# Kernel optimization log

Hardware: AMD Instinct MI355X
Metric: run time of the kernel (lower is better)

Reference implementation:

```python
import jax, jax.numpy as jnp
import numpy as np

B, T, D, H = 8, 4096, 1024, 1024


def log_g(x):
    # log of g(x) = relu(x)+0.5 for x>=0, sigmoid(x) for x<0 (continuous at 0)
    return jnp.where(x >= 0, jnp.log(jax.nn.relu(x) + 0.5), -jax.nn.softplus(-x))


def setup_inputs() -> dict:
    key = jax.random.key(0)
    k0, k1, k2, k3, k4, k5 = jax.random.split(key, 6)
    s = 1.0 / np.sqrt(D)
    return {
        "x": jax.random.normal(k0, (B, T, D), jnp.float32),
        "h_0": jax.random.normal(k1, (B, H), jnp.float32),
        "Wz": jax.random.uniform(k2, (H, D), jnp.float32, -s, s),
        "bz": jax.random.uniform(k3, (H,), jnp.float32, -s, s),
        "Wh": jax.random.uniform(k4, (H, D), jnp.float32, -s, s),
        "bh": jax.random.uniform(k5, (H,), jnp.float32, -s, s),
    }


def reference(x, h_0, Wz, bz, Wh, bh):
    # gate pre-activation k: (B,T,H)
    k = jnp.einsum("btd,hd->bth", x, Wz) + bz
    log_z = -jax.nn.softplus(-k)        # log sigmoid(k)
    log_coeffs = -jax.nn.softplus(k)    # log (1 - sigmoid(k))
    log_h_0 = log_g(h_0)[:, None, :]    # (B,1,H)
    log_tilde_h = log_g(jnp.einsum("btd,hd->bth", x, Wh) + bh)
    log_values = jnp.concatenate([log_h_0, log_z + log_tilde_h], axis=1)  # (B,T+1,H)
    # parallel scan in log space
    a_star = jnp.pad(jnp.cumsum(log_coeffs, axis=1), ((0, 0), (1, 0), (0, 0)))
    log_h = a_star + jax.lax.cumlogsumexp(log_values - a_star, axis=1)
    h = jnp.exp(log_h)                  # (B,T+1,H)
    return h[:, -T:, :]
```

## Files before the change

### kernel.cpp

```cpp
#include <hip/hip_runtime.h>
#include <hip/hip_bf16.h>

#define Bb 8
#define Tt 4096
#define Dd 1024
#define Hh 1024
#define Mm (Bb * Tt)
#define NCHUNK 32
#define CLEN 128

typedef float f32x4 __attribute__((ext_vector_type(4)));
typedef short bf16x8 __attribute__((ext_vector_type(8)));

__device__ __forceinline__ unsigned f2bfu(float x) {
  unsigned u = __float_as_uint(x);
  return (u + 0x7fffu + ((u >> 16) & 1u)) >> 16;
}
__device__ __forceinline__ float bflo(unsigned u) { return __uint_as_float(u << 16); }
__device__ __forceinline__ float bfhi(unsigned u) { return __uint_as_float(u & 0xffff0000u); }

#define NX4 (Mm * Dd / 4)
#define NW4 (Hh * Dd / 4)
__global__ void cvt_all_kernel(const float* __restrict__ x,
                               const float* __restrict__ wz,
                               const float* __restrict__ wh,
                               unsigned short* __restrict__ xb,
                               unsigned short* __restrict__ wzb,
                               unsigned short* __restrict__ whb) {
  const int n4 = NX4 + 2 * NW4;
  int i = blockIdx.x * blockDim.x + threadIdx.x;
  const int stride = gridDim.x * blockDim.x;
  for (; i < n4; i += stride) {
    const float* src;
    unsigned short* dst;
    int j = i;
    if (j < NX4) {
      src = x; dst = xb;
    } else if (j < NX4 + NW4) {
      j -= NX4; src = wz; dst = wzb;
    } else {
      j -= NX4 + NW4; src = wh; dst = whb;
    }
    float4 v = reinterpret_cast<const float4*>(src)[j];
    ushort4 o;
    o.x = (unsigned short)f2bfu(v.x);
    o.y = (unsigned short)f2bfu(v.y);
    o.z = (unsigned short)f2bfu(v.z);
    o.w = (unsigned short)f2bfu(v.w);
    reinterpret_cast<ushort4*>(dst)[j] = o;
  }
}

__device__ __forceinline__ void async16(const unsigned short* g, unsigned short* l) {
  __builtin_amdgcn_global_load_lds(
      (const __attribute__((address_space(1))) unsigned int*)g,
      (__attribute__((address_space(3))) unsigned int*)l, 16, 0, 0);
}

#define SHFL_COMPOSE(A, Q, MASK, HIBIT)                                   \
  {                                                                       \
    const float pA_ = __shfl_xor(A, MASK);                                \
    const float pQ_ = __shfl_xor(Q, MASK);                                \
    const float Alo_ = (HIBIT) ? pA_ : A;                                 \
    const float Qlo_ = (HIBIT) ? pQ_ : Q;                                 \
    const float Ahi_ = (HIBIT) ? A : pA_;                                 \
    const float Qhi_ = (HIBIT) ? Q : pQ_;                                 \
    A = Alo_ * Ahi_;                                                      \
    Q = fmaf(Ahi_, Qlo_, Qhi_);                                           \
  }

__global__ void __launch_bounds__(512, 4) gemm_kernel(
    const unsigned short* __restrict__ xb,
    const unsigned short* __restrict__ wzb,
    const unsigned short* __restrict__ whb,
    const float* __restrict__ bz,
    const float* __restrict__ bh,
    unsigned int* __restrict__ P,
    float* __restrict__ Pp, float* __restrict__ Qq) {
  __shared__ unsigned short lds[36864];
  const int tid = threadIdx.x;
  const int wid = tid >> 6;
  const int wm = wid >> 2;
  const int wn = wid & 3;
  const int l = tid & 63, ln = l & 15, l4 = l >> 4;

  const int id = blockIdx.x;
  const int sw = (id & 7) * 256 + (id >> 3);
  const int mb = sw >> 3, nb = sw & 7;
  const int m0 = mb * 128, h0 = nb * 128;

  const int r0 = tid >> 2;
  const int chunk = ((tid & 3) - (tid >> 3)) & 3;
  const unsigned short* agp = xb + (size_t)(m0 + r0) * Dd + chunk * 8;
  const int sub16 = r0 >> 4;
  const int hrow0 = h0 + ((sub16 >> 1) << 4) + (r0 & 15);
  const unsigned short* bgp =
      ((sub16 & 1) ? whb : wzb) + (size_t)hrow0 * Dd + chunk * 8;
  const int ta = tid * 8;

  auto stage = [&](int buf) {
    unsigned short* d = &lds[buf * 12288];
    async16(agp, d + ta);
    async16(bgp, d + 4096 + ta);
    async16(bgp + (size_t)64 * Dd, d + 8192 + ta);
    agp += 32;
    bgp += 32;
  };

  int oA[4], oB[4];
#pragma unroll
  for (int mf = 0; mf < 4; ++mf) {
    const int row = wm * 64 + mf * 16 + ln;
    const int sl = (l4 + (row >> 1)) & 3;
    oA[mf] = row * 32 + sl * 8;
  }
#pragma unroll
  for (int nf = 0; nf < 4; ++nf) {
    const int row = wn * 64 + nf * 16 + ln;
    const int sl = (l4 + (row >> 1)) & 3;
    oB[nf] = 4096 + row * 32 + sl * 8;
  }

  f32x4 acc[4][4];
#pragma unroll
  for (int i = 0; i < 4; ++i)
#pragma unroll
    for (int j = 0; j < 4; ++j) acc[i][j] = f32x4{0.f, 0.f, 0.f, 0.f};

  stage(0);
  stage(1);

  int cur = 0, nxt = 2;
#pragma unroll 1
  for (int s = 0; s < 32; ++s) {
    asm volatile("s_waitcnt vmcnt(3)" ::: "memory");
    __builtin_amdgcn_s_barrier();
    const unsigned short* bp = &lds[cur * 12288];
    bf16x8 af[4], bf[4];
    af[0] = *(const bf16x8*)(bp + oA[0]);
    af[1] = *(const bf16x8*)(bp + oA[1]);
    af[2] = *(const bf16x8*)(bp + oA[2]);
    af[3] = *(const bf16x8*)(bp + oA[3]);
    bf[0] = *(const bf16x8*)(bp + oB[0]);
    bf[1] = *(const bf16x8*)(bp + oB[1]);
    bf[2] = *(const bf16x8*)(bp + oB[2]);
    bf[3] = *(const bf16x8*)(bp + oB[3]);
    stage(nxt);
    __builtin_amdgcn_s_setprio(1);
#pragma unroll
    for (int i = 0; i < 4; ++i)
#pragma unroll
      for (int j = 0; j < 4; ++j)
        acc[i][j] =
            __builtin_amdgcn_mfma_f32_16x16x32_bf16(af[i], bf[j], acc[i][j], 0, 0, 0);
    __builtin_amdgcn_s_setprio(0);
    cur = (cur + 1) == 3 ? 0 : cur + 1;
    nxt = (nxt + 1) == 3 ? 0 : nxt + 1;
  }

  asm volatile("s_waitcnt vmcnt(0)" ::: "memory");
  __syncthreads();

  float* sA = (float*)lds;
  float* sQ = (float*)lds + 256;
  const int b_idx = mb >> 5;
  const int ch = mb & 31;

#pragma unroll
  for (int p = 0; p < 2; ++p) {
    const int hcol = h0 + (wn * 2 + p) * 16 + ln;
    const float bzv = bz[hcol];
    const float bhv = bh[hcol];
    float Ar = 1.f, Qr = 0.f;
#pragma unroll
    for (int mf = 0; mf < 4; ++mf) {
      float A4 = 1.f, Q4 = 0.f;
#pragma unroll
      for (int q = 0; q < 4; ++q) {
        const int m = m0 + wm * 64 + mf * 16 + l4 * 4 + q;
        const float kv = acc[mf][2 * p][q] + bzv;
        const float pv = acc[mf][2 * p + 1][q] + bhv;
        const float ek = __expf(kv);
        const float a = 1.f / (1.f + ek);
        const float z = 1.f - a;
        const float g = (pv >= 0.f) ? (pv + 0.5f) : (1.f / (1.f + __expf(-pv)));
        const float c = z * g;
        const unsigned pw = f2bfu(a) | (f2bfu(c) << 16);
        P[(size_t)m * Hh + hcol] = pw;
        const float ar = bflo(pw), cr = bfhi(pw);
        Q4 = fmaf(ar, Q4, cr);
        A4 *= ar;
      }
      SHFL_COMPOSE(A4, Q4, 16, (l4 & 1));
      SHFL_COMPOSE(A4, Q4, 32, ((l4 >> 1) & 1));
      Qr = fmaf(A4, Qr, Q4);
      Ar *= A4;
    }
    if (l4 == 0) {
      sA[wm * 128 + (wn * 2 + p) * 16 + ln] = Ar;
      sQ[wm * 128 + (wn * 2 + p) * 16 + ln] = Qr;
    }
  }
  __syncthreads();
  if (tid < 128) {
    const float A0 = sA[tid], Q0 = sQ[tid];
    const float A1 = sA[128 + tid], Q1 = sQ[128 + tid];
    const int idx = ch * (Bb * Hh) + b_idx * Hh + (h0 + tid);
    Pp[idx] = A0 * A1;
    Qq[idx] = fmaf(A1, Q0, Q1);
  }
}

__global__ void scan_pass2(const float* __restrict__ h0raw,
                           const float* __restrict__ Pp, const float* __restrict__ Qq,
                           float* __restrict__ Hinit) {
  const int bh = blockIdx.x * 256 + threadIdx.x;
  const float x = h0raw[bh];
  float hs = (x >= 0.f) ? (x + 0.5f) : (1.f / (1.f + __expf(-x)));
  for (int ch = 0; ch < NCHUNK; ++ch) {
    const int idx = ch * (Bb * Hh) + bh;
    Hinit[idx] = hs;
    hs = fmaf(Pp[idx], hs, Qq[idx]);
  }
}

__global__ void scan_pass3(const unsigned int* __restrict__ P,
                           const float* __restrict__ Hinit,
                           float* __restrict__ out) {
  const int h = blockIdx.x * 256 + threadIdx.x;
  const int ch = blockIdx.y;
  const int b = blockIdx.z;
  float hs = Hinit[ch * (Bb * Hh) + b * Hh + h];
  const size_t base = ((size_t)(b * Tt + ch * CLEN)) * Hh + h;
  const unsigned int* p = P + base;
  float* o = out + base;
#pragma unroll 8
  for (int i = 0; i < CLEN; ++i) {
    const unsigned u = p[(size_t)i * Hh];
    hs = fmaf(bflo(u), hs, bfhi(u));
    o[(size_t)i * Hh] = hs;
  }
}

extern "C" void kernel_launch(void* const* d_in, const int* in_sizes, int n_in,
                              void* d_out, int out_size, void* d_ws, size_t ws_size,
                              hipStream_t stream) {
  const float* x  = (const float*)d_in[0];
  const float* h0 = (const float*)d_in[1];
  const float* Wz = (const float*)d_in[2];
  const float* bz = (const float*)d_in[3];
  const float* Wh = (const float*)d_in[4];
  const float* bh = (const float*)d_in[5];
  float* out = (float*)d_out;

  char* ws = (char*)d_ws;
  unsigned short* xb  = (unsigned short*)(ws);
  unsigned short* wzb = (unsigned short*)(ws + 67108864);
  unsigned short* whb = (unsigned short*)(ws + 69206016);
  unsigned int*   P   = (unsigned int*)(ws + 71303168);
  float* Pp    = (float*)(ws + 205520896);
  float* Qq    = (float*)(ws + 206569472);
  float* Hinit = (float*)(ws + 207618048);

  cvt_all_kernel<<<4096, 256, 0, stream>>>(x, Wz, Wh, xb, wzb, whb);

  gemm_kernel<<<2048, 512, 0, stream>>>(xb, wzb, whb, bz, bh, P, Pp, Qq);

  scan_pass2<<<Bb * Hh / 256, 256, 0, stream>>>(h0, Pp, Qq, Hinit);
  dim3 sgrid(Hh / 256, NCHUNK, Bb);
  scan_pass3<<<sgrid, 256, 0, stream>>>(P, Hinit, out);
}
```

Before: 260.0 us.

## Fuse fp32-to-bf16 conversion of x into GEMM A-tile loading

Removes the separate conversion pass over x (128MB read plus 64MB bf16 write) and instead has the GEMM load fp32 x tiles into registers, convert them to bf16 and write them to LDS, while B tiles keep the async global-to-LDS path. Only the weights are converted in a small pre-kernel. The trade-off is that the GEMM now reads twice the A bytes (each fp32 x tile is read once per N-block, 8 times over), spends more VGPRs on in-flight loads (launch bounds lowered to 3 waves/SIMD), and adds register-staged LDS writes with waitcnt ordering in the main loop. At the tail the loop issues dummy loads from the first tile so the vmcnt accounting stays consistent.

```diff
diff --git a/kernel.cpp b/kernel.cpp
--- a/kernel.cpp
+++ b/kernel.cpp
@@ -19,28 +19,18 @@
 __device__ __forceinline__ float bflo(unsigned u) { return __uint_as_float(u << 16); }
 __device__ __forceinline__ float bfhi(unsigned u) { return __uint_as_float(u & 0xffff0000u); }
 
-#define NX4 (Mm * Dd / 4)
 #define NW4 (Hh * Dd / 4)
-__global__ void cvt_all_kernel(const float* __restrict__ x,
-                               const float* __restrict__ wz,
-                               const float* __restrict__ wh,
-                               unsigned short* __restrict__ xb,
-                               unsigned short* __restrict__ wzb,
-                               unsigned short* __restrict__ whb) {
-  const int n4 = NX4 + 2 * NW4;
+__global__ void cvt_w_kernel(const float* __restrict__ wz,
+                             const float* __restrict__ wh,
+                             unsigned short* __restrict__ wzb,
+                             unsigned short* __restrict__ whb) {
+  const int n4 = 2 * NW4;
   int i = blockIdx.x * blockDim.x + threadIdx.x;
   const int stride = gridDim.x * blockDim.x;
   for (; i < n4; i += stride) {
-    const float* src;
-    unsigned short* dst;
-    int j = i;
-    if (j < NX4) {
-      src = x; dst = xb;
-    } else if (j < NX4 + NW4) {
-      j -= NX4; src = wz; dst = wzb;
-    } else {
-      j -= NX4 + NW4; src = wh; dst = whb;
-    }
+    const float* src = (i < NW4) ? wz : wh;
+    unsigned short* dst = (i < NW4) ? wzb : whb;
+    const int j = (i < NW4) ? i : i - NW4;
     float4 v = reinterpret_cast<const float4*>(src)[j];
     ushort4 o;
     o.x = (unsigned short)f2bfu(v.x);
@@ -69,8 +59,8 @@
     Q = fmaf(Ahi_, Qlo_, Qhi_);                                           \
   }
 
-__global__ void __launch_bounds__(512, 4) gemm_kernel(
-    const unsigned short* __restrict__ xb,
+__global__ void __launch_bounds__(512, 3) gemm_kernel(
+    const float* __restrict__ x,
     const unsigned short* __restrict__ wzb,
     const unsigned short* __restrict__ whb,
     const float* __restrict__ bz,
@@ -91,20 +81,27 @@
 
   const int r0 = tid >> 2;
   const int chunk = ((tid & 3) - (tid >> 3)) & 3;
-  const unsigned short* agp = xb + (size_t)(m0 + r0) * Dd + chunk * 8;
+  const float* axbase = x + (size_t)(m0 + r0) * Dd + chunk * 8;
+  const float* axp = axbase;
   const int sub16 = r0 >> 4;
   const int hrow0 = h0 + ((sub16 >> 1) << 4) + (r0 & 15);
   const unsigned short* bgp =
       ((sub16 & 1) ? whb : wzb) + (size_t)hrow0 * Dd + chunk * 8;
   const int ta = tid * 8;
 
-  auto stage = [&](int buf) {
+  auto stageB = [&](int buf) {
     unsigned short* d = &lds[buf * 12288];
-    async16(agp, d + ta);
     async16(bgp, d + 4096 + ta);
     async16(bgp + (size_t)64 * Dd, d + 8192 + ta);
-    agp += 32;
     bgp += 32;
+  };
+  auto writeA = [&](int buf, const float4& v0, const float4& v1) {
+    uint4 w;
+    w.x = f2bfu(v0.x) | (f2bfu(v0.y) << 16);
+    w.y = f2bfu(v0.z) | (f2bfu(v0.w) << 16);
+    w.z = f2bfu(v1.x) | (f2bfu(v1.y) << 16);
+    w.w = f2bfu(v1.z) | (f2bfu(v1.w) << 16);
+    *reinterpret_cast<uint4*>(&lds[buf * 12288 + ta]) = w;
   };
 
   int oA[4], oB[4];
@@ -127,13 +124,25 @@
 #pragma unroll
     for (int j = 0; j < 4; ++j) acc[i][j] = f32x4{0.f, 0.f, 0.f, 0.f};
 
-  stage(0);
-  stage(1);
+  float4 av0, av1;
+
+  av0 = *(const float4*)(axp);
+  av1 = *(const float4*)(axp + 4);
+  axp += 32;
+  stageB(0);
+  asm volatile("s_waitcnt vmcnt(2)" ::: "memory");
+  writeA(0, av0, av1);
+  av0 = *(const float4*)(axp);
+  av1 = *(const float4*)(axp + 4);
+  axp += 32;
+  stageB(1);
+  asm volatile("s_waitcnt vmcnt(2)" ::: "memory");
+  writeA(1, av0, av1);
 
   int cur = 0, nxt = 2;
 #pragma unroll 1
   for (int s = 0; s < 32; ++s) {
-    asm volatile("s_waitcnt vmcnt(3)" ::: "memory");
+    asm volatile("s_waitcnt lgkmcnt(0)" ::: "memory");
     __builtin_amdgcn_s_barrier();
     const unsigned short* bp = &lds[cur * 12288];
     bf16x8 af[4], bf[4];
@@ -145,7 +154,11 @@
     bf[1] = *(const bf16x8*)(bp + oB[1]);
     bf[2] = *(const bf16x8*)(bp + oB[2]);
     bf[3] = *(const bf16x8*)(bp + oB[3]);
-    stage(nxt);
+    const float* ap = (s < 30) ? axp : axbase;
+    av0 = *(const float4*)(ap);
+    av1 = *(const float4*)(ap + 4);
+    axp += 32;
+    stageB(nxt);
     __builtin_amdgcn_s_setprio(1);
 #pragma unroll
     for (int i = 0; i < 4; ++i)
@@ -154,6 +167,8 @@
         acc[i][j] =
             __builtin_amdgcn_mfma_f32_16x16x32_bf16(af[i], bf[j], acc[i][j], 0, 0, 0);
     __builtin_amdgcn_s_setprio(0);
+    asm volatile("s_waitcnt vmcnt(2)" ::: "memory");
+    writeA(nxt, av0, av1);
     cur = (cur + 1) == 3 ? 0 : cur + 1;
     nxt = (nxt + 1) == 3 ? 0 : nxt + 1;
   }
@@ -254,7 +269,6 @@
   float* out = (float*)d_out;
 
   char* ws = (char*)d_ws;
-  unsigned short* xb  = (unsigned short*)(ws);
   unsigned short* wzb = (unsigned short*)(ws + 67108864);
   unsigned short* whb = (unsigned short*)(ws + 69206016);
   unsigned int*   P   = (unsigned int*)(ws + 71303168);
@@ -262,9 +276,9 @@
   float* Qq    = (float*)(ws + 206569472);
   float* Hinit = (float*)(ws + 207618048);
 
-  cvt_all_kernel<<<4096, 256, 0, stream>>>(x, Wz, Wh, xb, wzb, whb);
-
-  gemm_kernel<<<2048, 512, 0, stream>>>(xb, wzb, whb, bz, bh, P, Pp, Qq);
+  cvt_w_kernel<<<1024, 256, 0, stream>>>(Wz, Wh, wzb, whb);
+
+  gemm_kernel<<<2048, 512, 0, stream>>>(x, wzb, whb, bz, bh, P, Pp, Qq);
 
   scan_pass2<<<Bb * Hh / 256, 256, 0, stream>>>(h0, Pp, Qq, Hinit);
   dim3 sgrid(Hh / 256, NCHUNK, Bb);
```

Result: slower. 320.7 us (+23.4%).
